# Kernel tuning notes

Hardware: AMD Instinct MI355X
Metric: run time of the kernel (lower is better)

## Reference

```python
import jax, jax.numpy as jnp
import numpy as np

B, S, T = 4, 1024, 1024
CTX, QIN, C, H = 1024, 1024, 1024, 16
HD = C // H  # per-head channels


def setup_inputs() -> dict:
    key = jax.random.key(0)
    ks = jax.random.split(key, 12)
    s = 0.02
    return {
        "query": jax.random.normal(ks[0], (B, S, QIN), jnp.float32),
        "key": jax.random.normal(ks[1], (B, T, CTX), jnp.float32),
        "value": jax.random.normal(ks[2], (B, T, CTX), jnp.float32),
        "mask": jax.random.randint(ks[3], (B, S, T), 0, 2).astype(bool),
        "Wq": jax.random.normal(ks[4], (C, QIN), jnp.float32) * s,
        "bq": jax.random.normal(ks[5], (C,), jnp.float32) * s,
        "Wk": jax.random.normal(ks[6], (C, CTX), jnp.float32) * s,
        "bk": jax.random.normal(ks[7], (C,), jnp.float32) * s,
        "Wv": jax.random.normal(ks[8], (C, CTX), jnp.float32) * s,
        "bv": jax.random.normal(ks[9], (C,), jnp.float32) * s,
        "Wo": jax.random.normal(ks[10], (C, C), jnp.float32) * s,
        "bo": jax.random.normal(ks[11], (C,), jnp.float32) * s,
    }


def reference(query, key, value, mask, Wq, bq, Wk, bk, Wv, bv, Wo, bo):
    b, s, _ = query.shape
    t = key.shape[1]
    c = Wq.shape[0]
    h, hd = H, c // H
    q = (query @ Wq.T + bq).reshape(b, s, h, hd)
    k = (key @ Wk.T + bk).reshape(b, t, h, hd)
    v = (value @ Wv.T + bv).reshape(b, t, h, hd)
    # [B,H,S,T] scores, scaled by 1/sqrt(head_dim)
    score = jnp.einsum('bshd,bthd->bhst', q, k) * (hd ** -0.5)
    # masked_fill_(~mask[:, None, 0:1], -inf): mask key positions via row 0
    score = jnp.where(mask[:, None, 0:1], score, -jnp.inf)
    weights = jax.nn.softmax(score, axis=-1)
    out = jnp.einsum('bhst,bthd->bshd', weights, v).reshape(b, s, c)
    out = out @ Wo.T + bo
    out = out * mask[..., 0:1].astype(out.dtype)
    return out
```

## Files before the change

kernel.cpp:

```cpp
#include <hip/hip_runtime.h>
#include <stdint.h>

#define Bb  4
#define Ss  1024
#define Tt  1024
#define Cc  1024
#define Hh  16
#define HDd 64
#define Kk  1024

typedef __bf16 bf16;
typedef __bf16 bf16x8 __attribute__((ext_vector_type(8)));
typedef float  f32x4  __attribute__((ext_vector_type(4)));
typedef __attribute__((address_space(1))) uint32_t gu32;
typedef __attribute__((address_space(3))) uint32_t lu32;

__device__ __forceinline__ void load_lds16(const bf16* g, bf16* l) {
    __builtin_amdgcn_global_load_lds((gu32*)g, (lu32*)l, 16, 0, 0);
}

#define BARRIER_LDS() do {                                    \
    asm volatile("s_waitcnt lgkmcnt(0)" ::: "memory");        \
    __builtin_amdgcn_s_barrier();                             \
} while (0)

__global__ void cvt8(const float* __restrict__ s0, const float* __restrict__ s1,
                     const float* __restrict__ s2, const float* __restrict__ s3,
                     const float* __restrict__ s4, const float* __restrict__ s5,
                     const float* __restrict__ s6,
                     bf16* __restrict__ d0, bf16* __restrict__ d1,
                     bf16* __restrict__ d2, bf16* __restrict__ d3,
                     bf16* __restrict__ d4, bf16* __restrict__ d5,
                     bf16* __restrict__ d6)
{
    const float* s; bf16* d; int n;
    switch (blockIdx.y) {
        case 0: s = s0; d = d0; n = Bb * Ss * Kk; break;
        case 1: s = s1; d = d1; n = Bb * Ss * Kk; break;
        case 2: s = s2; d = d2; n = Bb * Ss * Kk; break;
        case 3: s = s3; d = d3; n = Cc * Kk; break;
        case 4: s = s4; d = d4; n = Cc * Kk; break;
        case 5: s = s5; d = d5; n = Cc * Kk; break;
        default: s = s6; d = d6; n = Cc * Kk; break;
    }
    const int i = (blockIdx.x * blockDim.x + threadIdx.x) * 8;
    if (i >= n) return;
    const float4 a = *(const float4*)(s + i);
    const float4 c = *(const float4*)(s + i + 4);
    bf16x8 o;
    o[0] = (bf16)a.x; o[1] = (bf16)a.y; o[2] = (bf16)a.z; o[3] = (bf16)a.w;
    o[4] = (bf16)c.x; o[5] = (bf16)c.y; o[6] = (bf16)c.z; o[7] = (bf16)c.w;
    *(bf16x8*)(d + i) = o;
}


__device__ __forceinline__ void mainloop_128x128(
    const bf16* __restrict__ Ab, const bf16* __restrict__ Wb,
    bf16* As, bf16* Bs, f32x4 acc[4][4])
{
    const int tid  = threadIdx.x;
    const int wid  = tid >> 6;
    const int lane = tid & 63;
    const int l16  = lane & 15;
    const int quad = lane >> 4;
    const int wm   = wid >> 1;
    const int wn   = wid & 1;
    const int r8   = lane >> 3;
    const int ssw  = ((lane & 7) ^ r8) * 8;

    for (int k0 = 0; k0 < Kk; k0 += 64) {
#pragma unroll
        for (int p = 0; p < 4; p++) {
            const int rb = wid * 32 + p * 8;
            load_lds16(Ab + (size_t)(rb + r8) * Kk + k0 + ssw, As + rb * 64);
            load_lds16(Wb + (size_t)(rb + r8) * Kk + k0 + ssw, Bs + rb * 64);
        }
        __syncthreads();
#pragma unroll
        for (int kh = 0; kh < 2; kh++) {
            bf16x8 af[4], bw[4];
#pragma unroll
            for (int i = 0; i < 4; i++)
                af[i] = *(const bf16x8*)(As + (wm * 64 + i * 16 + l16) * 64 +
                                         (((kh * 4 + quad) ^ (l16 & 7)) * 8));
#pragma unroll
            for (int j = 0; j < 4; j++)
                bw[j] = *(const bf16x8*)(Bs + (wn * 64 + j * 16 + l16) * 64 +
                                         (((kh * 4 + quad) ^ (l16 & 7)) * 8));
#pragma unroll
            for (int i = 0; i < 4; i++)
#pragma unroll
                for (int j = 0; j < 4; j++)
                    acc[i][j] = __builtin_amdgcn_mfma_f32_16x16x32_bf16(af[i], bw[j], acc[i][j], 0, 0, 0);
        }
        __syncthreads();
    }
}

__device__ __forceinline__ void mainloop_128x64(
    const bf16* __restrict__ Ab, const bf16* __restrict__ Wb,
    bf16* As, bf16* Bs, f32x4 acc[4][2])
{
    const int tid  = threadIdx.x;
    const int wid  = tid >> 6;
    const int lane = tid & 63;
    const int l16  = lane & 15;
    const int quad = lane >> 4;
    const int wm   = wid >> 1;
    const int wn   = wid & 1;
    const int r8   = lane >> 3;
    const int ssw  = ((lane & 7) ^ r8) * 8;

    for (int k0 = 0; k0 < Kk; k0 += 64) {
#pragma unroll
        for (int p = 0; p < 4; p++) {
            const int rb = wid * 32 + p * 8;
            load_lds16(Ab + (size_t)(rb + r8) * Kk + k0 + ssw, As + rb * 64);
        }
#pragma unroll
        for (int p = 0; p < 2; p++) {
            const int rb = wid * 16 + p * 8;
            load_lds16(Wb + (size_t)(rb + r8) * Kk + k0 + ssw, Bs + rb * 64);
        }
        __syncthreads();
#pragma unroll
        for (int kh = 0; kh < 2; kh++) {
            bf16x8 af[4], bw[2];
#pragma unroll
            for (int i = 0; i < 4; i++)
                af[i] = *(const bf16x8*)(As + (wm * 64 + i * 16 + l16) * 64 +
                                         (((kh * 4 + quad) ^ (l16 & 7)) * 8));
#pragma unroll
            for (int j = 0; j < 2; j++)
                bw[j] = *(const bf16x8*)(Bs + (wn * 32 + j * 16 + l16) * 64 +
                                         (((kh * 4 + quad) ^ (l16 & 7)) * 8));
#pragma unroll
            for (int i = 0; i < 4; i++)
#pragma unroll
                for (int j = 0; j < 2; j++)
                    acc[i][j] = __builtin_amdgcn_mfma_f32_16x16x32_bf16(af[i], bw[j], acc[i][j], 0, 0, 0);
        }
        __syncthreads();
    }
}

__global__ __launch_bounds__(256)
void gemm_qkv(const bf16* __restrict__ Aq, const bf16* __restrict__ Ak, const bf16* __restrict__ Av,
              const bf16* __restrict__ Wq, const bf16* __restrict__ Wk, const bf16* __restrict__ Wv,
              const float* __restrict__ bq, const float* __restrict__ bk, const float* __restrict__ bv,
              bf16* __restrict__ Oq, bf16* __restrict__ Ok, bf16* __restrict__ Ov)
{
    __shared__ __align__(16) bf16 As[128 * 64];
    __shared__ __align__(16) bf16 Bs[128 * 64];
    const int z = blockIdx.z;
    const bf16*  A    = (z == 0) ? Aq : (z == 1) ? Ak : Av;
    const bf16*  W    = (z == 0) ? Wq : (z == 1) ? Wk : Wv;
    const float* bias = (z == 0) ? bq : (z == 1) ? bk : bv;
    bf16*        O    = (z == 0) ? Oq : (z == 1) ? Ok : Ov;

    f32x4 acc[4][4];
    const f32x4 z4 = {0.f, 0.f, 0.f, 0.f};
#pragma unroll
    for (int i = 0; i < 4; i++)
#pragma unroll
        for (int j = 0; j < 4; j++) acc[i][j] = z4;

    mainloop_128x128(A + (size_t)blockIdx.x * 128 * Kk,
                     W + (size_t)blockIdx.y * 128 * Kk, As, Bs, acc);

    const int tid = threadIdx.x;
    const int wid = tid >> 6, lane = tid & 63;
    const int l16 = lane & 15, quad = lane >> 4;
    const int wm = wid >> 1, wn = wid & 1;
    const int row0 = blockIdx.x * 128 + wm * 64;
    const int col0 = blockIdx.y * 128 + wn * 64;
#pragma unroll
    for (int j = 0; j < 4; j++) {
        const int col = col0 + j * 16 + l16;
        const float bj = bias[col];
        const int h = col >> 6, d = col & 63;
#pragma unroll
        for (int i = 0; i < 4; i++) {
#pragma unroll
            for (int r = 0; r < 4; r++) {
                const int row = row0 + i * 16 + quad * 4 + r;
                const int b = row >> 10, s = row & 1023;
                const bf16 val = (bf16)(acc[i][j][r] + bj);
                if (z == 2) {
                    Ov[((size_t)((b * Hh + h) * HDd + d)) * Tt + s] = val;
                } else {
                    O[((size_t)(b * Hh + h) * Ss + s) * HDd + d] = val;
                }
            }
        }
    }
}

__global__ __launch_bounds__(256)
void gemm_out(const bf16* __restrict__ A, const bf16* __restrict__ W,
              const float* __restrict__ bias, const int* __restrict__ mask,
              float* __restrict__ out)
{
    __shared__ __align__(16) bf16 As[128 * 64];
    __shared__ __align__(16) bf16 Bs[64 * 64];
    f32x4 acc[4][2];
    const f32x4 z4 = {0.f, 0.f, 0.f, 0.f};
#pragma unroll
    for (int i = 0; i < 4; i++)
#pragma unroll
        for (int j = 0; j < 2; j++) acc[i][j] = z4;

    mainloop_128x64(A + (size_t)blockIdx.x * 128 * Kk,
                    W + (size_t)blockIdx.y * 64 * Kk, As, Bs, acc);

    const int tid = threadIdx.x;
    const int wid = tid >> 6, lane = tid & 63;
    const int l16 = lane & 15, quad = lane >> 4;
    const int wm = wid >> 1, wn = wid & 1;
    const int row0 = blockIdx.x * 128 + wm * 64;
    const int col0 = blockIdx.y * 64 + wn * 32;
#pragma unroll
    for (int j = 0; j < 2; j++) {
        const int col = col0 + j * 16 + l16;
        const float bj = bias[col];
#pragma unroll
        for (int i = 0; i < 4; i++) {
#pragma unroll
            for (int r = 0; r < 4; r++) {
                const int row = row0 + i * 16 + quad * 4 + r;
                const float mval = (mask[(size_t)row * Tt] != 0) ? 1.f : 0.f;
                out[(size_t)row * Cc + col] = (acc[i][j][r] + bj) * mval;
            }
        }
    }
}

__global__ __launch_bounds__(256, 4)
void attn(const bf16* __restrict__ Q, const bf16* __restrict__ Kp, const bf16* __restrict__ Vt,
          const int* __restrict__ mask, bf16* __restrict__ X)
{
    __shared__ __align__(16) bf16 Ks[64 * 64];
    __shared__ __align__(16) bf16 Vs[64 * 64];
    __shared__ __align__(16) bf16 Ps[4][16 * 72];
    const int g   = blockIdx.x;
    const int xcd = g & 7, idx = g >> 3;
    const int bh  = xcd * 8 + (idx >> 4);
    const int qblk = idx & 15;
    const int b = bh >> 4, h = bh & 15;
    const int tid = threadIdx.x, wid = tid >> 6, lane = tid & 63;
    const int l16 = lane & 15, quad = lane >> 4;
    const bf16* Qbh = Q  + (size_t)bh * Ss * HDd;
    const bf16* Kbh = Kp + (size_t)bh * Tt * HDd;
    const bf16* Vbh = Vt + (size_t)bh * HDd * Tt;
    const int*  mb  = mask + (size_t)b * Ss * Tt;
    const int q0 = qblk * 64 + wid * 16;
    bf16* Psw = &Ps[wid][0];

    const bf16x8 qf0 = *(const bf16x8*)(Qbh + (size_t)(q0 + l16) * HDd + quad * 8);
    const bf16x8 qf1 = *(const bf16x8*)(Qbh + (size_t)(q0 + l16) * HDd + 32 + quad * 8);

    float ls[4];
    f32x4 o[4];
    const f32x4 z4 = {0.f, 0.f, 0.f, 0.f};
#pragma unroll
    for (int r = 0; r < 4; r++) ls[r] = 0.f;
#pragma unroll
    for (int dblk = 0; dblk < 4; dblk++) o[dblk] = z4;

    const int srow = lane >> 3;
    const int schk = lane & 7;
    const int sswz = (schk ^ srow) * 8;
    const int c80 = wid * 2, c81 = wid * 2 + 1;

    const bf16* kg0 = Kbh + (size_t)(c80 * 8 + srow) * HDd + sswz;
    const bf16* kg1 = Kbh + (size_t)(c81 * 8 + srow) * HDd + sswz;
    const bf16* vg0 = Vbh + (size_t)(c80 * 8 + srow) * Tt + sswz;
    const bf16* vg1 = Vbh + (size_t)(c81 * 8 + srow) * Tt + sswz;
    bf16* kd0 = Ks + c80 * 512 + lane * 8;
    bf16* kd1 = Ks + c81 * 512 + lane * 8;
    bf16* vd0 = Vs + c80 * 512 + lane * 8;
    bf16* vd1 = Vs + c81 * 512 + lane * 8;

    bf16x8 ka0, ka1, va0, va1;
    bf16x8 kb0, kb1, vb0, vb1;
    int mA0, mA1, mA2, mA3, mB0, mB1, mB2, mB3;

#define LOADA(KT) do { const int _kt = (KT);                          \
    ka0 = *(const bf16x8*)(kg0 + (size_t)_kt * HDd);                  \
    ka1 = *(const bf16x8*)(kg1 + (size_t)_kt * HDd);                  \
    va0 = *(const bf16x8*)(vg0 + _kt);                                \
    va1 = *(const bf16x8*)(vg1 + _kt);                                \
    mA0 = mb[_kt + l16];      mA1 = mb[_kt + 16 + l16];               \
    mA2 = mb[_kt + 32 + l16]; mA3 = mb[_kt + 48 + l16]; } while (0)
#define LOADB(KT) do { const int _kt = (KT);                          \
    kb0 = *(const bf16x8*)(kg0 + (size_t)_kt * HDd);                  \
    kb1 = *(const bf16x8*)(kg1 + (size_t)_kt * HDd);                  \
    vb0 = *(const bf16x8*)(vg0 + _kt);                                \
    vb1 = *(const bf16x8*)(vg1 + _kt);                                \
    mB0 = mb[_kt + l16];      mB1 = mb[_kt + 16 + l16];               \
    mB2 = mb[_kt + 32 + l16]; mB3 = mb[_kt + 48 + l16]; } while (0)
#define STOREA() do {                                                 \
    *(bf16x8*)kd0 = ka0; *(bf16x8*)kd1 = ka1;                         \
    *(bf16x8*)vd0 = va0; *(bf16x8*)vd1 = va1; } while (0)
#define STOREB() do {                                                 \
    *(bf16x8*)kd0 = kb0; *(bf16x8*)kd1 = kb1;                         \
    *(bf16x8*)vd0 = vb0; *(bf16x8*)vd1 = vb1; } while (0)

    auto compute = [&](int m0, int m1, int m2, int m3) {
        f32x4 sc[4];
#pragma unroll
        for (int nb = 0; nb < 4; nb++) sc[nb] = z4;
#pragma unroll
        for (int nb = 0; nb < 4; nb++) {
            const bf16* krow = Ks + (nb * 16 + l16) * 64;
            const bf16x8 kf0 = *(const bf16x8*)(krow + ((quad       ^ (l16 & 7)) * 8));
            const bf16x8 kf1 = *(const bf16x8*)(krow + (((4 + quad) ^ (l16 & 7)) * 8));
            sc[nb] = __builtin_amdgcn_mfma_f32_16x16x32_bf16(qf0, kf0, sc[nb], 0, 0, 0);
            sc[nb] = __builtin_amdgcn_mfma_f32_16x16x32_bf16(qf1, kf1, sc[nb], 0, 0, 0);
        }

        const int mm[4] = {m0, m1, m2, m3};
#pragma unroll
        for (int nb = 0; nb < 4; nb++) {
            const float madd = mm[nb] ? 0.f : -1e30f;
#pragma unroll
            for (int r = 0; r < 4; r++) {
                const float p = __expf(sc[nb][r] * 0.125f + madd);
                ls[r] += p;
                Psw[(quad * 4 + r) * 72 + nb * 16 + l16] = (bf16)p;
            }
        }

#pragma unroll
        for (int kh = 0; kh < 2; kh++) {
            const bf16x8 pf = *(const bf16x8*)(Psw + l16 * 72 + kh * 32 + quad * 8);
#pragma unroll
            for (int dblk = 0; dblk < 4; dblk++) {
                const bf16x8 vf = *(const bf16x8*)(Vs + (dblk * 16 + l16) * 64 +
                                                   (((kh * 4 + quad) ^ (l16 & 7)) * 8));
                o[dblk] = __builtin_amdgcn_mfma_f32_16x16x32_bf16(pf, vf, o[dblk], 0, 0, 0);
            }
        }
    };

    LOADA(0);

    for (int kt = 0; kt < Tt; kt += 128) {
        BARRIER_LDS();
        LOADB(kt + 64);
        STOREA();
        BARRIER_LDS();
        compute(mA0, mA1, mA2, mA3);

        BARRIER_LDS();
        LOADA((kt + 128 < Tt) ? (kt + 128) : (Tt - 64));
        STOREB();
        BARRIER_LDS();
        compute(mB0, mB1, mB2, mB3);
    }
#undef LOADA
#undef LOADB
#undef STOREA
#undef STOREB

#pragma unroll
    for (int off = 1; off <= 8; off <<= 1)
#pragma unroll
        for (int r = 0; r < 4; r++)
            ls[r] += __shfl_xor(ls[r], off, 64);
    float inv[4];
#pragma unroll
    for (int r = 0; r < 4; r++) inv[r] = 1.f / ls[r];

#pragma unroll
    for (int dblk = 0; dblk < 4; dblk++) {
#pragma unroll
        for (int r = 0; r < 4; r++) {
            const int srow_q = q0 + quad * 4 + r;
            const int d = dblk * 16 + l16;
            X[(size_t)(b * Ss + srow_q) * Cc + h * HDd + d] = (bf16)(o[dblk][r] * inv[r]);
        }
    }
}

extern "C" void kernel_launch(void* const* d_in, const int* in_sizes, int n_in,
                              void* d_out, int out_size, void* d_ws, size_t ws_size,
                              hipStream_t stream)
{
    const float* query = (const float*)d_in[0];
    const float* key   = (const float*)d_in[1];
    const float* value = (const float*)d_in[2];
    const int*   mask  = (const int*)d_in[3];
    const float* Wq = (const float*)d_in[4];
    const float* bq = (const float*)d_in[5];
    const float* Wk = (const float*)d_in[6];
    const float* bk = (const float*)d_in[7];
    const float* Wv = (const float*)d_in[8];
    const float* bv = (const float*)d_in[9];
    const float* Wo = (const float*)d_in[10];
    const float* bo = (const float*)d_in[11];
    float* out = (float*)d_out;

    char* ws = (char*)d_ws;
    const size_t MB = 1024 * 1024;
    bf16* qb  = (bf16*)(ws + 0 * MB);
    bf16* kb  = (bf16*)(ws + 8 * MB);
    bf16* vb  = (bf16*)(ws + 16 * MB);
    bf16* wqb = (bf16*)(ws + 24 * MB);
    bf16* wkb = (bf16*)(ws + 26 * MB);
    bf16* wvb = (bf16*)(ws + 28 * MB);
    bf16* wob = (bf16*)(ws + 30 * MB);
    bf16* Qp  = (bf16*)(ws + 32 * MB);
    bf16* Kpp = (bf16*)(ws + 40 * MB);
    bf16* Vtp = (bf16*)(ws + 48 * MB);
    bf16* Xb  = (bf16*)(ws + 56 * MB);

    cvt8<<<dim3(2048, 7), 256, 0, stream>>>(query, key, value, Wq, Wk, Wv, Wo,
                                            qb, kb, vb, wqb, wkb, wvb, wob);
    gemm_qkv<<<dim3(32, 8, 3), 256, 0, stream>>>(qb, kb, vb, wqb, wkb, wvb,
                                                 bq, bk, bv, Qp, Kpp, Vtp);
    attn<<<dim3(1024), 256, 0, stream>>>(Qp, Kpp, Vtp, mask, Xb);
    gemm_out<<<dim3(32, 16), 256, 0, stream>>>(Xb, wob, bo, mask, out);
}
```

Measured before the change: 233.2 us.

## Double-buffer LDS in GEMM mainloop and shrink QKV tile to 128x64

```diff
diff --git a/kernel.cpp b/kernel.cpp
--- a/kernel.cpp
+++ b/kernel.cpp
@@ -21,6 +21,11 @@
 
 #define BARRIER_LDS() do {                                    \
     asm volatile("s_waitcnt lgkmcnt(0)" ::: "memory");        \
+    __builtin_amdgcn_s_barrier();                             \
+} while (0)
+
+#define BARRIER_VM() do {                                     \
+    asm volatile("s_waitcnt vmcnt(0)" ::: "memory");          \
     __builtin_amdgcn_s_barrier();                             \
 } while (0)
 
@@ -53,10 +58,9 @@
     *(bf16x8*)(d + i) = o;
 }
 
-
-__device__ __forceinline__ void mainloop_128x128(
+__device__ __forceinline__ void mainloop_128x64_2ph(
     const bf16* __restrict__ Ab, const bf16* __restrict__ Wb,
-    bf16* As, bf16* Bs, f32x4 acc[4][4])
+    bf16* As, bf16* Bs, f32x4 acc[4][2])
 {
     const int tid  = threadIdx.x;
     const int wid  = tid >> 6;
@@ -68,71 +72,32 @@
     const int r8   = lane >> 3;
     const int ssw  = ((lane & 7) ^ r8) * 8;
 
-    for (int k0 = 0; k0 < Kk; k0 += 64) {
+    auto stage = [&](int buf, int k0) {
+        bf16* Asb = As + buf * (128 * 64);
+        bf16* Bsb = Bs + buf * (64 * 64);
 #pragma unroll
         for (int p = 0; p < 4; p++) {
             const int rb = wid * 32 + p * 8;
-            load_lds16(Ab + (size_t)(rb + r8) * Kk + k0 + ssw, As + rb * 64);
-            load_lds16(Wb + (size_t)(rb + r8) * Kk + k0 + ssw, Bs + rb * 64);
-        }
-        __syncthreads();
-#pragma unroll
-        for (int kh = 0; kh < 2; kh++) {
-            bf16x8 af[4], bw[4];
-#pragma unroll
-            for (int i = 0; i < 4; i++)
-                af[i] = *(const bf16x8*)(As + (wm * 64 + i * 16 + l16) * 64 +
-                                         (((kh * 4 + quad) ^ (l16 & 7)) * 8));
-#pragma unroll
-            for (int j = 0; j < 4; j++)
-                bw[j] = *(const bf16x8*)(Bs + (wn * 64 + j * 16 + l16) * 64 +
-                                         (((kh * 4 + quad) ^ (l16 & 7)) * 8));
-#pragma unroll
-            for (int i = 0; i < 4; i++)
-#pragma unroll
-                for (int j = 0; j < 4; j++)
-                    acc[i][j] = __builtin_amdgcn_mfma_f32_16x16x32_bf16(af[i], bw[j], acc[i][j], 0, 0, 0);
-        }
-        __syncthreads();
-    }
-}
-
-__device__ __forceinline__ void mainloop_128x64(
-    const bf16* __restrict__ Ab, const bf16* __restrict__ Wb,
-    bf16* As, bf16* Bs, f32x4 acc[4][2])
-{
-    const int tid  = threadIdx.x;
-    const int wid  = tid >> 6;
-    const int lane = tid & 63;
-    const int l16  = lane & 15;
-    const int quad = lane >> 4;
-    const int wm   = wid >> 1;
-    const int wn   = wid & 1;
-    const int r8   = lane >> 3;
-    const int ssw  = ((lane & 7) ^ r8) * 8;
-
-    for (int k0 = 0; k0 < Kk; k0 += 64) {
-#pragma unroll
-        for (int p = 0; p < 4; p++) {
-            const int rb = wid * 32 + p * 8;
-            load_lds16(Ab + (size_t)(rb + r8) * Kk + k0 + ssw, As + rb * 64);
+            load_lds16(Ab + (size_t)(rb + r8) * Kk + k0 + ssw, Asb + rb * 64);
         }
 #pragma unroll
         for (int p = 0; p < 2; p++) {
             const int rb = wid * 16 + p * 8;
-            load_lds16(Wb + (size_t)(rb + r8) * Kk + k0 + ssw, Bs + rb * 64);
-        }
-        __syncthreads();
+            load_lds16(Wb + (size_t)(rb + r8) * Kk + k0 + ssw, Bsb + rb * 64);
+        }
+    };
+
+    auto compute = [&](const bf16* Asb, const bf16* Bsb) {
 #pragma unroll
         for (int kh = 0; kh < 2; kh++) {
             bf16x8 af[4], bw[2];
 #pragma unroll
             for (int i = 0; i < 4; i++)
-                af[i] = *(const bf16x8*)(As + (wm * 64 + i * 16 + l16) * 64 +
+                af[i] = *(const bf16x8*)(Asb + (wm * 64 + i * 16 + l16) * 64 +
                                          (((kh * 4 + quad) ^ (l16 & 7)) * 8));
 #pragma unroll
             for (int j = 0; j < 2; j++)
-                bw[j] = *(const bf16x8*)(Bs + (wn * 32 + j * 16 + l16) * 64 +
+                bw[j] = *(const bf16x8*)(Bsb + (wn * 32 + j * 16 + l16) * 64 +
                                          (((kh * 4 + quad) ^ (l16 & 7)) * 8));
 #pragma unroll
             for (int i = 0; i < 4; i++)
@@ -140,7 +105,18 @@
                 for (int j = 0; j < 2; j++)
                     acc[i][j] = __builtin_amdgcn_mfma_f32_16x16x32_bf16(af[i], bw[j], acc[i][j], 0, 0, 0);
         }
-        __syncthreads();
+    };
+
+    stage(0, 0);
+    BARRIER_VM();
+
+    for (int k0 = 0; k0 < Kk; k0 += 128) {
+        stage(1, k0 + 64);
+        compute(As, Bs);
+        BARRIER_VM();
+        if (k0 + 128 < Kk) stage(0, k0 + 128);
+        compute(As + 128 * 64, Bs + 64 * 64);
+        BARRIER_VM();
     }
 }
 
@@ -150,32 +126,32 @@
               const float* __restrict__ bq, const float* __restrict__ bk, const float* __restrict__ bv,
               bf16* __restrict__ Oq, bf16* __restrict__ Ok, bf16* __restrict__ Ov)
 {
-    __shared__ __align__(16) bf16 As[128 * 64];
-    __shared__ __align__(16) bf16 Bs[128 * 64];
+    __shared__ __align__(16) bf16 As[2 * 128 * 64];
+    __shared__ __align__(16) bf16 Bs[2 * 64 * 64];
     const int z = blockIdx.z;
     const bf16*  A    = (z == 0) ? Aq : (z == 1) ? Ak : Av;
     const bf16*  W    = (z == 0) ? Wq : (z == 1) ? Wk : Wv;
     const float* bias = (z == 0) ? bq : (z == 1) ? bk : bv;
     bf16*        O    = (z == 0) ? Oq : (z == 1) ? Ok : Ov;
 
-    f32x4 acc[4][4];
+    f32x4 acc[4][2];
     const f32x4 z4 = {0.f, 0.f, 0.f, 0.f};
 #pragma unroll
     for (int i = 0; i < 4; i++)
 #pragma unroll
-        for (int j = 0; j < 4; j++) acc[i][j] = z4;
-
-    mainloop_128x128(A + (size_t)blockIdx.x * 128 * Kk,
-                     W + (size_t)blockIdx.y * 128 * Kk, As, Bs, acc);
+        for (int j = 0; j < 2; j++) acc[i][j] = z4;
+
+    mainloop_128x64_2ph(A + (size_t)blockIdx.x * 128 * Kk,
+                        W + (size_t)blockIdx.y * 64 * Kk, As, Bs, acc);
 
     const int tid = threadIdx.x;
     const int wid = tid >> 6, lane = tid & 63;
     const int l16 = lane & 15, quad = lane >> 4;
     const int wm = wid >> 1, wn = wid & 1;
     const int row0 = blockIdx.x * 128 + wm * 64;
-    const int col0 = blockIdx.y * 128 + wn * 64;
-#pragma unroll
-    for (int j = 0; j < 4; j++) {
+    const int col0 = blockIdx.y * 64 + wn * 32;
+#pragma unroll
+    for (int j = 0; j < 2; j++) {
         const int col = col0 + j * 16 + l16;
         const float bj = bias[col];
         const int h = col >> 6, d = col & 63;
@@ -201,8 +177,8 @@
               const float* __restrict__ bias, const int* __restrict__ mask,
               float* __restrict__ out)
 {
-    __shared__ __align__(16) bf16 As[128 * 64];
-    __shared__ __align__(16) bf16 Bs[64 * 64];
+    __shared__ __align__(16) bf16 As[2 * 128 * 64];
+    __shared__ __align__(16) bf16 Bs[2 * 64 * 64];
     f32x4 acc[4][2];
     const f32x4 z4 = {0.f, 0.f, 0.f, 0.f};
 #pragma unroll
@@ -210,8 +186,8 @@
 #pragma unroll
         for (int j = 0; j < 2; j++) acc[i][j] = z4;
 
-    mainloop_128x64(A + (size_t)blockIdx.x * 128 * Kk,
-                    W + (size_t)blockIdx.y * 64 * Kk, As, Bs, acc);
+    mainloop_128x64_2ph(A + (size_t)blockIdx.x * 128 * Kk,
+                        W + (size_t)blockIdx.y * 64 * Kk, As, Bs, acc);
 
     const int tid = threadIdx.x;
     const int wid = tid >> 6, lane = tid & 63;
@@ -417,8 +393,8 @@
 
     cvt8<<<dim3(2048, 7), 256, 0, stream>>>(query, key, value, Wq, Wk, Wv, Wo,
                                             qb, kb, vb, wqb, wkb, wvb, wob);
-    gemm_qkv<<<dim3(32, 8, 3), 256, 0, stream>>>(qb, kb, vb, wqb, wkb, wvb,
-                                                 bq, bk, bv, Qp, Kpp, Vtp);
+    gemm_qkv<<<dim3(32, 16, 3), 256, 0, stream>>>(qb, kb, vb, wqb, wkb, wvb,
+                                                  bq, bk, bv, Qp, Kpp, Vtp);
     attn<<<dim3(1024), 256, 0, stream>>>(Qp, Kpp, Vtp, mask, Xb);
     gemm_out<<<dim3(32, 16), 256, 0, stream>>>(Xb, wob, bo, mask, out);
 }
```

Result: no change. 232.6 us (-0.3%).
